# Kernel optimization log

Hardware: AMD Instinct MI355X
Metric: run time of the kernel (lower is better)

The kernel has to match this reference:

```python
import math
import jax, jax.numpy as jnp
import numpy as np


def setup_inputs() -> dict:
    key = jax.random.key(0)
    ks = jax.random.split(key, 5)
    B, N, D, O = 16, 16384, 256, 256
    x = jax.random.normal(ks[0], (B, N, D), dtype=jnp.float32)
    Wq = jax.random.normal(ks[1], (O, D), dtype=jnp.float32) * (1.0 / math.sqrt(D))
    bq = jax.random.normal(ks[2], (O,), dtype=jnp.float32) * 0.01
    Wk = jax.random.normal(ks[3], (O, D), dtype=jnp.float32) * (1.0 / math.sqrt(D))
    bk = jax.random.normal(ks[4], (O,), dtype=jnp.float32) * 0.01
    return {"x": x, "Wq": Wq, "bq": bq, "Wk": Wk, "bk": bk}


def reference(x, Wq, bq, Wk, bk):
    # x: [B, N, D]; Wq/Wk: [O, D] (torch nn.Linear layout), bq/bk: [O]
    O = Wq.shape[0]
    scale = 1.0 / math.sqrt(O)
    q = jnp.einsum('bnd,od->bno', x, Wq) + bq          # [B, N, O]
    k = jnp.einsum('bnd,od->bno', x, Wk) + bk          # [B, N, O]
    # sum_j (q_i . k_j) == q_i . (sum_j k_j): avoid the O(N^2) score matrix
    ksum = k.sum(axis=1)                               # [B, O]
    summed_scores = jnp.einsum('bno,bo->bn', q, ksum) * scale  # [B, N]
    customer_weights = jax.nn.softmax(summed_scores, axis=-1)  # [B, N]
    aggregated_feature = jnp.einsum('bn,bnd->bd', customer_weights, x)  # [B, D]
    average_customer_weights = customer_weights.mean(axis=0)            # [N]
    return aggregated_feature, average_customer_weights
```

## Files before the change

### kernel.cpp

```cpp
#include <hip/hip_runtime.h>
#include <math.h>

#define BB 16
#define NN 16384
#define DD 256
#define NS1 128
#define NS3 128

__global__ __launch_bounds__(256) void k1_xsum_part(const float* __restrict__ x,
                                                    float* __restrict__ part) {
  const int b = blockIdx.y, blk = blockIdx.x;
  const int wave = threadIdx.x >> 6, lane = threadIdx.x & 63;
  const int rows = NN / NS1;
  const float* xp = x + ((size_t)b * NN + (size_t)blk * rows) * DD;
  float4 acc = make_float4(0.f, 0.f, 0.f, 0.f);
  for (int r = wave; r < rows; r += 4) {
    float4 v = *(const float4*)(xp + (size_t)r * DD + lane * 4);
    acc.x += v.x; acc.y += v.y; acc.z += v.z; acc.w += v.w;
  }
  __shared__ float sP[4][DD];
  *(float4*)&sP[wave][lane * 4] = acc;
  __syncthreads();
  const int t = threadIdx.x;
  part[((size_t)b * NS1 + blk) * DD + t] = sP[0][t] + sP[1][t] + sP[2][t] + sP[3][t];
}

__global__ __launch_bounds__(256) void k2_prep(const float* __restrict__ part,
                                               const float* __restrict__ Wq,
                                               const float* __restrict__ bq,
                                               const float* __restrict__ Wk,
                                               const float* __restrict__ bk,
                                               float* __restrict__ v,
                                               float* __restrict__ c) {
  const int b = blockIdx.x, t = threadIdx.x;
  __shared__ float xs[DD];
  __shared__ float ks[DD];
  __shared__ float red[256];

  float acc = 0.f;
  for (int blk = 0; blk < NS1; ++blk) acc += part[((size_t)b * NS1 + blk) * DD + t];
  xs[t] = acc;
  __syncthreads();

  float kacc = (float)NN * bk[t];
  const float4* wkrow4 = (const float4*)(Wk + (size_t)t * DD);
#pragma unroll 4
  for (int j4 = 0; j4 < DD / 4; ++j4) {
    const float4 w = wkrow4[j4];
    kacc += w.x * xs[4 * j4] + w.y * xs[4 * j4 + 1] + w.z * xs[4 * j4 + 2] + w.w * xs[4 * j4 + 3];
  }
  ks[t] = kacc;
  __syncthreads();

  float vacc = 0.f;
  for (int o = 0; o < DD; ++o) vacc += Wq[(size_t)o * DD + t] * ks[o];
  v[b * DD + t] = vacc;

  red[t] = bq[t] * ks[t];
  __syncthreads();
  for (int s = 128; s > 0; s >>= 1) {
    if (t < s) red[t] += red[t + s];
    __syncthreads();
  }
  if (t == 0) c[b] = red[0];
}

__global__ __launch_bounds__(256) void k3_main(const float* __restrict__ x,
                                               const float* __restrict__ v,
                                               const float* __restrict__ c,
                                               float* __restrict__ scores,
                                               float* __restrict__ pm,
                                               float* __restrict__ pz,
                                               float* __restrict__ pP) {
  const int b = BB - 1 - blockIdx.y;
  const int blk = NS3 - 1 - blockIdx.x;
  const int wave = threadIdx.x >> 6, lane = threadIdx.x & 63;
  const float scale = 0.0625f;

  const float4 vl = *(const float4*)(v + b * DD + lane * 4);
  const float cb = c[b];
  const int rows_per_block = NN / NS3;
  const int rows_per_wave = rows_per_block / 4;
  const int n0 = blk * rows_per_block + wave * rows_per_wave;
  const float* xb = x + (size_t)b * NN * DD;

  float m = -INFINITY, Z = 0.f;
  float4 P = make_float4(0.f, 0.f, 0.f, 0.f);

  for (int i = 0; i < rows_per_wave; ++i) {
    const int n = n0 + i;
    float4 xr = *(const float4*)(xb + (size_t)n * DD + lane * 4);
    float dot = xr.x * vl.x + xr.y * vl.y + xr.z * vl.z + xr.w * vl.w;
#pragma unroll
    for (int off = 32; off >= 1; off >>= 1) dot += __shfl_xor(dot, off, 64);
    const float s = (dot + cb) * scale;
    if (lane == 0) scores[(size_t)b * NN + n] = s;

    const float mn = fmaxf(m, s);
    const float alpha = __expf(m - mn);
    const float e = __expf(s - mn);
    Z = Z * alpha + e;
    P.x = P.x * alpha + e * xr.x;
    P.y = P.y * alpha + e * xr.y;
    P.z = P.z * alpha + e * xr.z;
    P.w = P.w * alpha + e * xr.w;
    m = mn;
  }

  __shared__ float sm[4], sz[4];
  __shared__ float sP[4][DD];
  *(float4*)&sP[wave][lane * 4] = P;
  if (lane == 0) { sm[wave] = m; sz[wave] = Z; }
  __syncthreads();

  const int t = threadIdx.x;
  const float M = fmaxf(fmaxf(sm[0], sm[1]), fmaxf(sm[2], sm[3]));
  const float e0 = __expf(sm[0] - M), e1 = __expf(sm[1] - M);
  const float e2 = __expf(sm[2] - M), e3 = __expf(sm[3] - M);
  const float Pd = sP[0][t] * e0 + sP[1][t] * e1 + sP[2][t] * e2 + sP[3][t] * e3;
  const size_t idx = (size_t)b * NS3 + blk;
  pP[idx * DD + t] = Pd;
  if (t == 0) {
    pm[idx] = M;
    pz[idx] = sz[0] * e0 + sz[1] * e1 + sz[2] * e2 + sz[3] * e3;
  }
}

__global__ __launch_bounds__(256) void k45_final(const float* __restrict__ pm,
                                                 const float* __restrict__ pz,
                                                 const float* __restrict__ pP,
                                                 const float* __restrict__ scores,
                                                 float* __restrict__ out_agg,
                                                 float* __restrict__ out_w) {
  const int t = threadIdx.x;
  if (blockIdx.x < BB) {
    const int b = blockIdx.x;
    __shared__ float red[256];
    const size_t base = (size_t)b * NS3;

    red[t] = (t < NS3) ? pm[base + t] : -INFINITY;
    __syncthreads();
    for (int s = 128; s > 0; s >>= 1) {
      if (t < s) red[t] = fmaxf(red[t], red[t + s]);
      __syncthreads();
    }
    const float M = red[0];
    __syncthreads();

    red[t] = (t < NS3) ? pz[base + t] * __expf(pm[base + t] - M) : 0.f;
    __syncthreads();
    for (int s = 128; s > 0; s >>= 1) {
      if (t < s) red[t] += red[t + s];
      __syncthreads();
    }
    const float rZ = 1.f / red[0];

    float acc = 0.f;
    for (int blk = 0; blk < NS3; ++blk)
      acc += pP[(base + blk) * DD + t] * __expf(pm[base + blk] - M);
    out_agg[b * DD + t] = acc * rZ;
  } else {
    const int wb = blockIdx.x - BB;
    __shared__ float sM[BB], sR[BB];
    const int b = t >> 4;
    const int i = t & 15;
    const size_t base = (size_t)b * NS3 + i * 8;

    float mloc = -INFINITY;
#pragma unroll
    for (int k = 0; k < 8; ++k) mloc = fmaxf(mloc, pm[base + k]);
#pragma unroll
    for (int off = 8; off >= 1; off >>= 1) mloc = fmaxf(mloc, __shfl_xor(mloc, off, 64));
    const float M = mloc;

    float zloc = 0.f;
#pragma unroll
    for (int k = 0; k < 8; ++k) zloc += pz[base + k] * __expf(pm[base + k] - M);
#pragma unroll
    for (int off = 8; off >= 1; off >>= 1) zloc += __shfl_xor(zloc, off, 64);

    if (i == 0) { sM[b] = M; sR[b] = 1.f / zloc; }
    __syncthreads();

    const int n = wb * 256 + t;
    float acc = 0.f;
#pragma unroll
    for (int bb = 0; bb < BB; ++bb)
      acc += __expf(scores[(size_t)bb * NN + n] - sM[bb]) * sR[bb];
    out_w[n] = acc * (1.f / BB);
  }
}

extern "C" void kernel_launch(void* const* d_in, const int* in_sizes, int n_in,
                              void* d_out, int out_size, void* d_ws, size_t ws_size,
                              hipStream_t stream) {
  const float* x  = (const float*)d_in[0];
  const float* Wq = (const float*)d_in[1];
  const float* bq = (const float*)d_in[2];
  const float* Wk = (const float*)d_in[3];
  const float* bk = (const float*)d_in[4];

  float* out  = (float*)d_out;
  float* agg  = out;
  float* avgw = out + BB * DD;

  float* ws = (float*)d_ws;
  float* part   = ws;  ws += (size_t)BB * NS1 * DD;
  float* v      = ws;  ws += BB * DD;
  float* c      = ws;  ws += BB;
  float* scores = ws;  ws += (size_t)BB * NN;
  float* pm     = ws;  ws += BB * NS3;
  float* pz     = ws;  ws += BB * NS3;
  float* pP     = ws;  ws += (size_t)BB * NS3 * DD;

  k1_xsum_part<<<dim3(NS1, BB), 256, 0, stream>>>(x, part);
  k2_prep<<<BB, 256, 0, stream>>>(part, Wq, bq, Wk, bk, v, c);
  k3_main<<<dim3(NS3, BB), 256, 0, stream>>>(x, v, c, scores, pm, pz, pP);
  k45_final<<<BB + NN / 256, 256, 0, stream>>>(pm, pz, pP, scores, agg, avgw);
}
```

Baseline: 119.5 us.

## Split batch in halves and overlap x-sum of second half with main pass of first

```diff
diff --git a/kernel.cpp b/kernel.cpp
--- a/kernel.cpp
+++ b/kernel.cpp
@@ -6,10 +6,11 @@
 #define DD 256
 #define NS1 128
 #define NS3 128
-
-__global__ __launch_bounds__(256) void k1_xsum_part(const float* __restrict__ x,
-                                                    float* __restrict__ part) {
-  const int b = blockIdx.y, blk = blockIdx.x;
+#define GB 8
+
+__device__ __forceinline__ void xsum_partial_body(const float* __restrict__ x,
+                                                  float* __restrict__ part,
+                                                  int b, int blk) {
   const int wave = threadIdx.x >> 6, lane = threadIdx.x & 63;
   const int rows = NN / NS1;
   const float* xp = x + ((size_t)b * NN + (size_t)blk * rows) * DD;
@@ -18,21 +19,26 @@
     float4 v = *(const float4*)(xp + (size_t)r * DD + lane * 4);
     acc.x += v.x; acc.y += v.y; acc.z += v.z; acc.w += v.w;
   }
-  __shared__ float sP[4][DD];
-  *(float4*)&sP[wave][lane * 4] = acc;
+  __shared__ float sQ[4][DD];
+  *(float4*)&sQ[wave][lane * 4] = acc;
   __syncthreads();
   const int t = threadIdx.x;
-  part[((size_t)b * NS1 + blk) * DD + t] = sP[0][t] + sP[1][t] + sP[2][t] + sP[3][t];
-}
-
-__global__ __launch_bounds__(256) void k2_prep(const float* __restrict__ part,
-                                               const float* __restrict__ Wq,
-                                               const float* __restrict__ bq,
-                                               const float* __restrict__ Wk,
-                                               const float* __restrict__ bk,
-                                               float* __restrict__ v,
-                                               float* __restrict__ c) {
-  const int b = blockIdx.x, t = threadIdx.x;
+  part[((size_t)b * NS1 + blk) * DD + t] = sQ[0][t] + sQ[1][t] + sQ[2][t] + sQ[3][t];
+}
+
+__global__ __launch_bounds__(256) void kA(const float* __restrict__ x,
+                                          float* __restrict__ part, int b0) {
+  xsum_partial_body(x, part, b0 + blockIdx.y, blockIdx.x);
+}
+
+__global__ __launch_bounds__(256) void kB(const float* __restrict__ part,
+                                          const float* __restrict__ Wq,
+                                          const float* __restrict__ bq,
+                                          const float* __restrict__ Wk,
+                                          const float* __restrict__ bk,
+                                          float* __restrict__ v,
+                                          float* __restrict__ c, int b0) {
+  const int b = b0 + blockIdx.x, t = threadIdx.x;
   __shared__ float xs[DD];
   __shared__ float ks[DD];
   __shared__ float red[256];
@@ -65,15 +71,31 @@
   if (t == 0) c[b] = red[0];
 }
 
-__global__ __launch_bounds__(256) void k3_main(const float* __restrict__ x,
-                                               const float* __restrict__ v,
-                                               const float* __restrict__ c,
-                                               float* __restrict__ scores,
-                                               float* __restrict__ pm,
-                                               float* __restrict__ pz,
-                                               float* __restrict__ pP) {
-  const int b = BB - 1 - blockIdx.y;
-  const int blk = NS3 - 1 - blockIdx.x;
+__global__ __launch_bounds__(256) void kC(const float* __restrict__ x,
+                                          const float* __restrict__ v,
+                                          const float* __restrict__ c,
+                                          float* __restrict__ part,
+                                          float* __restrict__ scores,
+                                          float* __restrict__ pm,
+                                          float* __restrict__ pz,
+                                          float* __restrict__ pP,
+                                          int b0A, int b0B) {
+  int role, local;
+  if (b0B >= 0) {
+    role = (blockIdx.x >> 3) & 1;
+    local = (int)(((blockIdx.x >> 4) << 3) | (blockIdx.x & 7));
+  } else {
+    role = 0;
+    local = blockIdx.x;
+  }
+
+  if (role) {
+    xsum_partial_body(x, part, b0B + (local >> 7), local & (NS1 - 1));
+    return;
+  }
+
+  const int b = b0A + (local >> 7);
+  const int blk = local & (NS3 - 1);
   const int wave = threadIdx.x >> 6, lane = threadIdx.x & 63;
   const float scale = 0.0625f;
 
@@ -213,8 +235,10 @@
   float* pz     = ws;  ws += BB * NS3;
   float* pP     = ws;  ws += (size_t)BB * NS3 * DD;
 
-  k1_xsum_part<<<dim3(NS1, BB), 256, 0, stream>>>(x, part);
-  k2_prep<<<BB, 256, 0, stream>>>(part, Wq, bq, Wk, bk, v, c);
-  k3_main<<<dim3(NS3, BB), 256, 0, stream>>>(x, v, c, scores, pm, pz, pP);
+  kA<<<dim3(NS1, GB), 256, 0, stream>>>(x, part, 0);
+  kB<<<GB, 256, 0, stream>>>(part, Wq, bq, Wk, bk, v, c, 0);
+  kC<<<2 * GB * NS3, 256, 0, stream>>>(x, v, c, part, scores, pm, pz, pP, 0, GB);
+  kB<<<GB, 256, 0, stream>>>(part, Wq, bq, Wk, bk, v, c, GB);
+  kC<<<GB * NS3, 256, 0, stream>>>(x, v, c, part, scores, pm, pz, pP, GB, -1);
   k45_final<<<BB + NN / 256, 256, 0, stream>>>(pm, pz, pP, scores, agg, avgw);
 }
```

Measured after the change: 141.8 us. +18.6%, slower.
